# Kernel tuning notes

Measured on AMD Instinct MI355X. Metric: run time of the kernel, lower is better.

Reference implementation:

```python
import jax, jax.numpy as jnp
import numpy as np

B, K, C, D, L, H, FF = 64, 1024, 512, 256, 2, 4, 1024
DH = D // H
EPS = 1e-5
NEG = -jnp.inf
SCALE = 1.0 / float(np.sqrt(DH))


def _ln(x, w, b):
    m = x.mean(-1, keepdims=True)
    v = ((x - m) ** 2).mean(-1, keepdims=True)
    return (x - m) * jax.lax.rsqrt(v + EPS) * w + b


def _star_attn(x, key_pad, pad_c, Wq, bq, Wk, bk, Wv, bv, Wo, bo):
    # Star topology: rows 0,1 (query,dustbin) attend to all non-padded keys;
    # each candidate row attends only to {query, dustbin, itself}.
    Bb, S, _ = x.shape
    q = (x @ Wq.T + bq).reshape(Bb, S, H, DH)
    k = (x @ Wk.T + bk).reshape(Bb, S, H, DH)
    v = (x @ Wv.T + bv).reshape(Bb, S, H, DH)
    # global rows
    qg = q[:, :2]
    sg = jnp.einsum('bthd,bshd->bhts', qg, k) * SCALE            # [B,H,2,S]
    sg = jnp.where(key_pad[:, None, None, :], NEG, sg)
    out_g = jnp.einsum('bhts,bshd->bthd', jax.nn.softmax(sg, -1), v)  # [B,2,H,DH]
    # candidate rows: scores against the 2 global keys + self key
    qc, kc, vc = q[:, 2:], k[:, 2:], v[:, 2:]
    kg, vg = k[:, :2], v[:, :2]
    s2 = jnp.einsum('bkhd,bthd->bkht', qc, kg) * SCALE           # [B,K,H,2]
    ss = jnp.einsum('bkhd,bkhd->bkh', qc, kc) * SCALE            # [B,K,H]
    ss = jnp.where(pad_c[:, :, None], NEG, ss)                   # padded self-key disallowed
    w = jax.nn.softmax(jnp.concatenate([s2, ss[..., None]], -1), -1)  # [B,K,H,3]
    out_c = jnp.einsum('bkht,bthd->bkhd', w[..., :2], vg) + w[..., 2:] * vc
    out = jnp.concatenate([out_g, out_c], 1).reshape(Bb, S, D)
    return out @ Wo.T + bo


def _forward(query, candidates, candidate_mask, qp_w, qp_b, cp_w, cp_b,
             dustbin, type_emb, ln1_w, ln1_b, ln2_w, ln2_b,
             Wq, bq, Wk, bk, Wv, bv, Wo, bo,
             ff1_w, ff1_b, ff2_w, ff2_b, head_ln_w, head_ln_b, head_w, head_b):
    Bb = query.shape[0]
    qt = (query @ qp_w.T + qp_b + type_emb[0])[:, None]          # [B,1,D]
    dt = jnp.broadcast_to(dustbin + type_emb[1], (Bb, 1, D))
    ct = candidates @ cp_w.T + cp_b + type_emb[2]                # [B,K,D]
    x = jnp.concatenate([qt, dt, ct], 1)                         # [B,K+2,D]
    pad_c = jnp.logical_not(candidate_mask)
    key_pad = jnp.concatenate([jnp.zeros((Bb, 2), bool), pad_c], 1)
    for l in range(L):  # pre-LN encoder layers (norm_first, eval so dropout=0)
        x = x + _star_attn(_ln(x, ln1_w[l], ln1_b[l]), key_pad, pad_c,
                           Wq[l], bq[l], Wk[l], bk[l], Wv[l], bv[l], Wo[l], bo[l])
        h = _ln(x, ln2_w[l], ln2_b[l])
        x = x + (jax.nn.gelu(h @ ff1_w[l].T + ff1_b[l], approximate=False) @ ff2_w[l].T + ff2_b[l])
    logits = (_ln(x, head_ln_w, head_ln_b) @ head_w.T + head_b)[..., 0]  # [B,K+2]
    cand = jnp.where(candidate_mask, logits[:, 2:], NEG)
    return jnp.concatenate([logits[:, 1:2], cand], 1)            # [B,K+1]


def setup_inputs() -> dict:
    key = jax.random.key(0)
    ks = iter(jax.random.split(key, 40))
    n = lambda shape, s=0.02: jax.random.normal(next(ks), shape, jnp.float32) * s
    return dict(
        query=jax.random.normal(next(ks), (B, C), jnp.float32),
        candidates=jax.random.normal(next(ks), (B, K, C), jnp.float32),
        candidate_mask=jax.random.bernoulli(next(ks), 0.9, (B, K)),
        qp_w=n((D, C)), qp_b=jnp.zeros(D),
        cp_w=n((D, C)), cp_b=jnp.zeros(D),
        dustbin=n((D,)), type_emb=n((3, D)),
        ln1_w=jnp.ones((L, D)), ln1_b=jnp.zeros((L, D)),
        ln2_w=jnp.ones((L, D)), ln2_b=jnp.zeros((L, D)),
        Wq=n((L, D, D)), bq=jnp.zeros((L, D)),
        Wk=n((L, D, D)), bk=jnp.zeros((L, D)),
        Wv=n((L, D, D)), bv=jnp.zeros((L, D)),
        Wo=n((L, D, D)), bo=jnp.zeros((L, D)),
        ff1_w=n((L, FF, D)), ff1_b=jnp.zeros((L, FF)),
        ff2_w=n((L, D, FF)), ff2_b=jnp.zeros((L, D)),
        head_ln_w=jnp.ones(D), head_ln_b=jnp.zeros(D),
        head_w=n((1, D)), head_b=jnp.zeros(1),
    )


def reference(query, candidates, candidate_mask, qp_w, qp_b, cp_w, cp_b,
              dustbin, type_emb, ln1_w, ln1_b, ln2_w, ln2_b,
              Wq, bq, Wk, bk, Wv, bv, Wo, bo,
              ff1_w, ff1_b, ff2_w, ff2_b, head_ln_w, head_ln_b, head_w, head_b):
    return _forward(query, candidates, candidate_mask, qp_w, qp_b, cp_w, cp_b,
                    dustbin, type_emb, ln1_w, ln1_b, ln2_w, ln2_b,
                    Wq, bq, Wk, bk, Wv, bv, Wo, bo,
                    ff1_w, ff1_b, ff2_w, ff2_b, head_ln_w, head_ln_b, head_w, head_b)
```

## Files before the change

### kernel.cpp

```cpp
#include <hip/hip_runtime.h>
#include <math.h>

static constexpr int Bc = 64;
static constexpr int Kc = 1024;
static constexpr int Cc = 512;
static constexpr int Dc = 256;
static constexpr int Hc = 4;
static constexpr int Sc = 1026;
static constexpr int FFc = 1024;
static constexpr float EPSc = 1e-5f;
static constexpr float SCALEc = 0.125f;
static constexpr float NEG_OUT = -1.0e30f;

typedef __attribute__((ext_vector_type(8))) short short8;
typedef __attribute__((ext_vector_type(8))) unsigned short u16x8;
typedef __attribute__((ext_vector_type(4))) float f32x4;

__device__ __forceinline__ float bf2f(unsigned short u) {
  union { float f; unsigned int i; } c; c.i = ((unsigned int)u) << 16; return c.f;
}
__device__ __forceinline__ unsigned short f2bf(float f) {
  union { float f; unsigned int i; } c; c.f = f;
  unsigned int i = c.i;
  unsigned int r = (i + 0x7fffu + ((i >> 16) & 1u)) >> 16;
  return (unsigned short)r;
}
__device__ __forceinline__ unsigned int cvt_pk_bf16(float a, float b) {
  unsigned int d;
  asm("v_cvt_pk_bf16_f32 %0, %1, %2" : "=v"(d) : "v"(a), "v"(b));
  return d;
}

__device__ __forceinline__ float wave_sum(float v) {
#pragma unroll
  for (int off = 32; off > 0; off >>= 1) v += __shfl_xor(v, off, 64);
  return v;
}
__device__ __forceinline__ float wave_max(float v) {
#pragma unroll
  for (int off = 32; off > 0; off >>= 1) v = fmaxf(v, __shfl_xor(v, off, 64));
  return v;
}

__device__ __forceinline__ void async_ld16(const unsigned short* g, unsigned short* l) {
  __builtin_amdgcn_global_load_lds(
      (const __attribute__((address_space(1))) void*)g,
      (__attribute__((address_space(3))) void*)l, 16, 0, 0);
}

__device__ __forceinline__ float gelu_fast(float u) {
  const float z = u * fmaf(u * u, 0.07135481627f, 1.5957691216f);
  return __fdividef(u, 1.0f + __expf(-z));
}

template <int EPI, int MAP, int CASTA>
__global__ __launch_bounds__(256) void gemm_mfma(
    const void* __restrict__ Av, const unsigned short* __restrict__ W,
    const float* __restrict__ bias, const void* extra,
    void* Cout, int N, int Kd, int ldc, int MB, int NB) {
  __shared__ unsigned short lds[24576];
  const int xcd = blockIdx.x & 7;
  const int slot = blockIdx.x >> 3;
  const int nb = slot % NB;
  const int mb = (slot / NB) * 8 + xcd;
  if (mb >= MB) return;
  const int m0 = mb * 128;
  const int n0 = nb * 128;
  const int tid = threadIdx.x;
  const int w = tid >> 6;
  const int lane = tid & 63;

  const unsigned short* A = (const unsigned short*)Av;
  const float* Af = (const float*)Av;

  const int srA[2] = {(w * 2 + 0) * 16 + (lane >> 2), (w * 2 + 1) * 16 + (lane >> 2)};
  const unsigned short* pA[2];
  const unsigned short* pB[2];
#pragma unroll
  for (int c = 0; c < 2; ++c) {
    const int kc = ((lane & 3) ^ ((srA[c] >> 1) & 3)) * 8;
    if (!CASTA) pA[c] = A + (size_t)(m0 + srA[c]) * Kd + kc;
    pB[c] = W + (size_t)(n0 + srA[c]) * Kd + kc;
  }
  const int lreg0 = (w * 2 + 0) * 512;
  const int lreg1 = (w * 2 + 1) * 512;

  f32x4 zero = {0.f, 0.f, 0.f, 0.f};
  f32x4 acc[4][4];
#pragma unroll
  for (int i = 0; i < 4; ++i)
#pragma unroll
    for (int j = 0; j < 4; ++j) acc[i][j] = zero;

  const int mrow = (w & 1) * 64;
  const int nrow = (w >> 1) * 64;
  const int l15 = lane & 15;
  const int quad = lane >> 4;
  const int koff = (quad ^ ((l15 >> 1) & 3)) * 16;

  auto stage = [&](int kk, int b) {
    if (CASTA) {
#pragma unroll
      for (int wi = 0; wi < 4; ++wi) {
        const int g = wi * 256 + tid;
        const int row = g >> 3;
        const int k4 = g & 7;
        const int phys =
            row * 32 + ((((k4 >> 1) ^ ((row >> 1) & 3))) << 3) + ((k4 & 1) << 2);
        const float4 a4 =
            *(const float4*)(Af + (size_t)(m0 + row) * Kd + kk + k4 * 4);
        uint2 o;
        o.x = cvt_pk_bf16(a4.x, a4.y);
        o.y = cvt_pk_bf16(a4.z, a4.w);
        *(uint2*)(&lds[b * 4096 + phys]) = o;
      }
    } else {
      async_ld16(pA[0] + kk, &lds[b * 4096 + lreg0]);
      async_ld16(pA[1] + kk, &lds[b * 4096 + lreg1]);
    }
    async_ld16(pB[0] + kk, &lds[12288 + b * 4096 + lreg0]);
    async_ld16(pB[1] + kk, &lds[12288 + b * 4096 + lreg1]);
  };

  auto compute_tile = [&](int cur) {
    const char* AsB = (const char*)&lds[cur * 4096];
    const char* WsB = (const char*)&lds[12288 + cur * 4096];
    short8 af[4], bfr[4];
#pragma unroll
    for (int i = 0; i < 4; ++i)
      af[i] = *(const short8*)(AsB + (size_t)(mrow + i * 16 + l15) * 64 + koff);
#pragma unroll
    for (int j = 0; j < 4; ++j)
      bfr[j] = *(const short8*)(WsB + (size_t)(nrow + j * 16 + l15) * 64 + koff);
#pragma unroll
    for (int i = 0; i < 4; ++i)
#pragma unroll
      for (int j = 0; j < 4; ++j)
        acc[i][j] = __builtin_amdgcn_mfma_f32_16x16x32_bf16(bfr[j], af[i],
                                                            acc[i][j], 0, 0, 0);
  };

  const int niter = Kd >> 5;
  if (CASTA) {
    stage(0, 0);
    for (int it = 0; it < niter; ++it) {
      const int cur = it & 1;
      __syncthreads();
      if (it + 1 < niter) stage((it + 1) << 5, cur ^ 1);
      compute_tile(cur);
    }
  } else {
    stage(0, 0);
    stage(32, 1);
    int cur = 0;
    for (int it = 0; it < niter; ++it) {
      if (it + 1 < niter)
        asm volatile("s_waitcnt vmcnt(4)" ::: "memory");
      else
        asm volatile("s_waitcnt vmcnt(0)" ::: "memory");
      asm volatile("s_waitcnt lgkmcnt(0)" ::: "memory");
      __builtin_amdgcn_s_barrier();
      if (it + 2 < niter) {
        int b2 = cur + 2; if (b2 >= 3) b2 -= 3;
        stage((it + 2) << 5, b2);
      }
      compute_tile(cur);
      cur = (cur == 2) ? 0 : cur + 1;
    }
  }

  const float* extraF = (const float*)extra;
  const unsigned short* extraB = (const unsigned short*)extra;
  float4 bj[4];
#pragma unroll
  for (int j = 0; j < 4; ++j) {
    const int n = n0 + nrow + j * 16 + quad * 4;
    float4 t4 = *(const float4*)(bias + n);
    if (EPI == 1) {
      const float4 e4 = *(const float4*)(extraF + n);
      t4.x += e4.x; t4.y += e4.y; t4.z += e4.z; t4.w += e4.w;
    }
    bj[j] = t4;
  }
  __syncthreads();
#pragma unroll
  for (int i = 0; i < 4; ++i) {
    const int m = mrow + i * 16 + l15;
    const int swz = (m & 7) << 1;
#pragma unroll
    for (int j = 0; j < 4; ++j) {
      float v0 = acc[i][j][0] + bj[j].x;
      float v1 = acc[i][j][1] + bj[j].y;
      float v2 = acc[i][j][2] + bj[j].z;
      float v3 = acc[i][j][3] + bj[j].w;
      if (EPI == 3) {
        v0 = gelu_fast(v0); v1 = gelu_fast(v1);
        v2 = gelu_fast(v2); v3 = gelu_fast(v3);
      }
      uint2 pk;
      pk.x = cvt_pk_bf16(v0, v1);
      pk.y = cvt_pk_bf16(v2, v3);
      const int g = ((nrow + j * 16 + quad * 4) >> 2) ^ swz;
      *(uint2*)(&lds[m * 128 + g * 4]) = pk;
    }
  }
  __syncthreads();
  unsigned short* outb = (unsigned short*)Cout;
#pragma unroll
  for (int c8 = 0; c8 < 8; ++c8) {
    const int idx = c8 * 256 + tid;
    const int row = idx >> 4;
    const int cc = idx & 15;
    const int gsr = (2 * cc) ^ ((row & 7) << 1);
    u16x8 val = *(const u16x8*)(&lds[row * 128 + gsr * 4]);
    const int col = cc * 8;
    const int m = m0 + row;
    const size_t orow =
        (MAP == 1) ? ((size_t)(m >> 10) * Sc + 2 + (m & 1023)) : (size_t)m;
    const size_t go = orow * (size_t)ldc + n0 + col;
    if (EPI == 2) {
      u16x8 rv = *(const u16x8*)(extraB + go);
      unsigned int* vp = (unsigned int*)&val;
#pragma unroll
      for (int e = 0; e < 4; ++e) {
        const float a0 = bf2f(val[2 * e]) + bf2f(rv[2 * e]);
        const float a1 = bf2f(val[2 * e + 1]) + bf2f(rv[2 * e + 1]);
        vp[e] = cvt_pk_bf16(a0, a1);
      }
    }
    *(u16x8*)(outb + go) = val;
  }
}

struct CastTab {
  const float* src[10];
  unsigned short* dst[10];
  int n4[10];
};
__global__ __launch_bounds__(256) void cast_multi(CastTab t) {
  const int e = blockIdx.y;
  const int n4 = t.n4[e];
  const float4* s = (const float4*)t.src[e];
  uint2* d = (uint2*)t.dst[e];
  for (int i = blockIdx.x * 256 + threadIdx.x; i < n4; i += gridDim.x * 256) {
    float4 f = s[i];
    uint2 o;
    o.x = cvt_pk_bf16(f.x, f.y);
    o.y = cvt_pk_bf16(f.z, f.w);
    d[i] = o;
  }
}

__global__ __launch_bounds__(256) void bias_concat(const float* bq, const float* bk,
                                                   const float* bv, float* qkvb) {
  const int i = blockIdx.x * 256 + threadIdx.x;
  if (i >= 2 * 768) return;
  const int l = i / 768;
  const int j = i - l * 768;
  float v;
  if (j < 256) v = bq[l * 256 + j];
  else if (j < 512) v = bk[l * 256 + j - 256];
  else v = bv[l * 256 + j - 512];
  qkvb[i] = v;
}

__global__ __launch_bounds__(256) void embed_qd(
    const float* __restrict__ qin, const float* __restrict__ qp_w,
    const float* __restrict__ qp_b, const float* __restrict__ dustbin,
    const float* __restrict__ type_emb, unsigned short* __restrict__ x) {
  const int b = blockIdx.x;
  const int d = threadIdx.x;
  __shared__ __align__(16) float qs[512];
  qs[d] = qin[b * 512 + d];
  qs[d + 256] = qin[b * 512 + 256 + d];
  __syncthreads();
  float acc = 0.0f;
  const float* wr = qp_w + (size_t)d * 512;
#pragma unroll 4
  for (int c = 0; c < 512; c += 4) {
    float4 w4 = *(const float4*)(wr + c);
    acc = fmaf(qs[c], w4.x, acc);
    acc = fmaf(qs[c + 1], w4.y, acc);
    acc = fmaf(qs[c + 2], w4.z, acc);
    acc = fmaf(qs[c + 3], w4.w, acc);
  }
  const size_t base = (size_t)b * Sc * Dc;
  x[base + d] = f2bf(acc + qp_b[d] + type_emb[d]);
  x[base + Dc + d] = f2bf(dustbin[d] + type_emb[Dc + d]);
}

__global__ __launch_bounds__(256) void ln_kernel(
    const unsigned short* __restrict__ x, const float* __restrict__ w,
    const float* __restrict__ b, unsigned short* __restrict__ y, int nrows) {
  const int wave = threadIdx.x >> 6;
  const int lane = threadIdx.x & 63;
  const int row0 = blockIdx.x * 16 + wave * 4;
  const float4 wv = *(const float4*)(w + lane * 4);
  const float4 bv = *(const float4*)(b + lane * 4);
#pragma unroll
  for (int r = 0; r < 4; ++r) {
    const int row = row0 + r;
    if (row >= nrows) return;
    const unsigned short* xr = x + (size_t)row * Dc;
    ushort4 xv = *(const ushort4*)(xr + lane * 4);
    const float v0 = bf2f(xv.x), v1 = bf2f(xv.y), v2 = bf2f(xv.z), v3 = bf2f(xv.w);
    float s = v0 + v1 + v2 + v3;
    float sq = v0 * v0 + v1 * v1 + v2 * v2 + v3 * v3;
    s = wave_sum(s);
    sq = wave_sum(sq);
    const float mean = s * (1.0f / Dc);
    const float var = sq * (1.0f / Dc) - mean * mean;
    const float rs = rsqrtf(var + EPSc);
    uint2 o;
    o.x = cvt_pk_bf16((v0 - mean) * rs * wv.x + bv.x,
                      (v1 - mean) * rs * wv.y + bv.y);
    o.y = cvt_pk_bf16((v2 - mean) * rs * wv.z + bv.z,
                      (v3 - mean) * rs * wv.w + bv.w);
    *(uint2*)(y + (size_t)row * Dc + lane * 4) = o;
  }
}

__global__ __launch_bounds__(256) void attn_global(
    const unsigned short* __restrict__ qkv, const unsigned char* __restrict__ mask,
    unsigned short* __restrict__ ao) {
  const int b = blockIdx.x;
  const int h = blockIdx.y;
  const int tid = threadIdx.x;
  const int wv = tid >> 6;
  const int lane = tid & 63;
  __shared__ float q0s[64], q1s[64];
  __shared__ float sc0[Sc], sc1[Sc];
  __shared__ float rbuf[4][2];
  __shared__ float obuf[2][4][64];
  const size_t base = (size_t)b * Sc * 768 + h * 64;
  if (tid < 64) {
    q0s[tid] = bf2f(qkv[base + tid]);
    q1s[tid] = bf2f(qkv[base + 768 + tid]);
  }
  __syncthreads();

  float lm0 = -INFINITY, lm1 = -INFINITY;
  for (int s = tid; s < Sc; s += 256) {
    const unsigned short* kr = qkv + base + 256 + (size_t)s * 768;
    float d0 = 0.0f, d1 = 0.0f;
#pragma unroll
    for (int c = 0; c < 64; c += 8) {
      u16x8 kv = *(const u16x8*)(kr + c);
#pragma unroll
      for (int e = 0; e < 8; ++e) {
        const float kf = bf2f(kv[e]);
        d0 = fmaf(q0s[c + e], kf, d0);
        d1 = fmaf(q1s[c + e], kf, d1);
      }
    }
    const bool pad = (s >= 2) && (mask[b * Kc + (s - 2)] == 0);
    const float s0 = pad ? -INFINITY : d0 * SCALEc;
    const float s1 = pad ? -INFINITY : d1 * SCALEc;
    sc0[s] = s0; sc1[s] = s1;
    lm0 = fmaxf(lm0, s0); lm1 = fmaxf(lm1, s1);
  }
  lm0 = wave_max(lm0);
  lm1 = wave_max(lm1);
  if (lane == 0) { rbuf[wv][0] = lm0; rbuf[wv][1] = lm1; }
  __syncthreads();
  const float m0 = fmaxf(fmaxf(rbuf[0][0], rbuf[1][0]), fmaxf(rbuf[2][0], rbuf[3][0]));
  const float m1 = fmaxf(fmaxf(rbuf[0][1], rbuf[1][1]), fmaxf(rbuf[2][1], rbuf[3][1]));
  float ls0 = 0.0f, ls1 = 0.0f;
  for (int s = tid; s < Sc; s += 256) {
    const float e0 = expf(sc0[s] - m0);
    const float e1 = expf(sc1[s] - m1);
    sc0[s] = e0; sc1[s] = e1;
    ls0 += e0; ls1 += e1;
  }
  ls0 = wave_sum(ls0);
  ls1 = wave_sum(ls1);
  __syncthreads();
  if (lane == 0) { rbuf[wv][0] = ls0; rbuf[wv][1] = ls1; }
  __syncthreads();
  const float t0 = rbuf[0][0] + rbuf[1][0] + rbuf[2][0] + rbuf[3][0];
  const float t1 = rbuf[0][1] + rbuf[1][1] + rbuf[2][1] + rbuf[3][1];
  float o0 = 0.0f, o1 = 0.0f;
  for (int s = wv; s < Sc; s += 4) {
    const float vvv = bf2f(qkv[base + 512 + (size_t)s * 768 + lane]);
    o0 = fmaf(sc0[s], vvv, o0);
    o1 = fmaf(sc1[s], vvv, o1);
  }
  obuf[0][wv][lane] = o0;
  obuf[1][wv][lane] = o1;
  __syncthreads();
  if (wv == 0) {
    const float a0 = obuf[0][0][lane] + obuf[0][1][lane] + obuf[0][2][lane] + obuf[0][3][lane];
    const float a1 = obuf[1][0][lane] + obuf[1][1][lane] + obuf[1][2][lane] + obuf[1][3][lane];
    const size_t ob = ((size_t)b * Sc) * Dc + h * 64;
    ao[ob + lane] = f2bf(a0 / t0);
    ao[ob + Dc + lane] = f2bf(a1 / t1);
  }
}

__global__ __launch_bounds__(256) void attn_cand(
    const unsigned short* __restrict__ qkv, const unsigned char* __restrict__ mask,
    unsigned short* __restrict__ ao) {
  const int b = blockIdx.x >> 3;
  const int k0 = (blockIdx.x & 7) << 7;
  const int h = threadIdx.x >> 6;
  const int lane = threadIdx.x & 63;
  const int c4 = lane >> 4;
  const int l16 = lane & 15;
  const size_t bbase = (size_t)b * Sc * 768;
  const unsigned short* gp = qkv + bbase + h * 64 + l16 * 4;
  float k0f[4], k1f[4], v0f[4], v1f[4];
  {
    const ushort4 a = *(const ushort4*)(gp + 256);
    const ushort4 c = *(const ushort4*)(gp + 256 + 768);
    const ushort4 d = *(const ushort4*)(gp + 512);
    const ushort4 e = *(const ushort4*)(gp + 512 + 768);
    k0f[0] = bf2f(a.x); k0f[1] = bf2f(a.y); k0f[2] = bf2f(a.z); k0f[3] = bf2f(a.w);
    k1f[0] = bf2f(c.x); k1f[1] = bf2f(c.y); k1f[2] = bf2f(c.z); k1f[3] = bf2f(c.w);
    v0f[0] = bf2f(d.x); v0f[1] = bf2f(d.y); v0f[2] = bf2f(d.z); v0f[3] = bf2f(d.w);
    v1f[0] = bf2f(e.x); v1f[1] = bf2f(e.y); v1f[2] = bf2f(e.z); v1f[3] = bf2f(e.w);
  }
  for (int t = 0; t < 32; ++t) {
    const int kk = k0 + t * 4 + c4;
    const unsigned short* cp =
        qkv + bbase + (size_t)(2 + kk) * 768 + h * 64 + l16 * 4;
    const ushort4 qv = *(const ushort4*)cp;
    const ushort4 kv = *(const ushort4*)(cp + 256);
    const ushort4 vv = *(const ushort4*)(cp + 512);
    const unsigned short* qp = (const unsigned short*)&qv;
    const unsigned short* kp = (const unsigned short*)&kv;
    const unsigned short* vp = (const unsigned short*)&vv;
    float p0 = 0.f, p1 = 0.f, p2 = 0.f;
#pragma unroll
    for (int e = 0; e < 4; ++e) {
      const float qf = bf2f(qp[e]);
      p0 = fmaf(qf, k0f[e], p0);
      p1 = fmaf(qf, k1f[e], p1);
      p2 = fmaf(qf, bf2f(kp[e]), p2);
    }
#pragma unroll
    for (int off = 1; off < 16; off <<= 1) {
      p0 += __shfl_xor(p0, off, 64);
      p1 += __shfl_xor(p1, off, 64);
      p2 += __shfl_xor(p2, off, 64);
    }
    const bool pad = (mask[b * Kc + kk] == 0);
    const float s0 = p0 * SCALEc;
    const float s1 = p1 * SCALEc;
    const float s2 = pad ? -INFINITY : p2 * SCALEc;
    const float m = fmaxf(fmaxf(s0, s1), s2);
    const float e0 = expf(s0 - m);
    const float e1 = expf(s1 - m);
    const float e2 = pad ? 0.0f : expf(s2 - m);
    const float inv = 1.0f / (e0 + e1 + e2);
    float o[4];
#pragma unroll
    for (int e = 0; e < 4; ++e)
      o[e] = (e0 * v0f[e] + e1 * v1f[e] + e2 * bf2f(vp[e])) * inv;
    uint2 pk;
    pk.x = cvt_pk_bf16(o[0], o[1]);
    pk.y = cvt_pk_bf16(o[2], o[3]);
    *(uint2*)(ao + ((size_t)b * Sc + 2 + kk) * Dc + h * 64 + l16 * 4) = pk;
  }
}

__global__ __launch_bounds__(256) void head_kernel(
    const unsigned short* __restrict__ x, const float* __restrict__ lnw,
    const float* __restrict__ lnb, const float* __restrict__ hw,
    const float* __restrict__ hb, const unsigned char* __restrict__ mask,
    float* __restrict__ out) {
  const int lane = threadIdx.x & 63;
  const int gw0 = blockIdx.x * 16 + (threadIdx.x >> 6) * 4;
  const float4 wv = *(const float4*)(lnw + lane * 4);
  const float4 bv = *(const float4*)(lnb + lane * 4);
  const float4 hv = *(const float4*)(hw + lane * 4);
  const float hb0 = hb[0];
#pragma unroll
  for (int r = 0; r < 4; ++r) {
    const int gw = gw0 + r;
    if (gw >= Bc * 1025) return;
    const int b = gw / 1025;
    const int j = gw - b * 1025;
    const int s = 1 + j;
    const unsigned short* xr = x + ((size_t)b * Sc + s) * Dc;
    ushort4 xv = *(const ushort4*)(xr + lane * 4);
    const float v0 = bf2f(xv.x), v1 = bf2f(xv.y), v2 = bf2f(xv.z), v3 = bf2f(xv.w);
    float su = v0 + v1 + v2 + v3;
    float sq = v0 * v0 + v1 * v1 + v2 * v2 + v3 * v3;
    su = wave_sum(su);
    sq = wave_sum(sq);
    const float mean = su * (1.0f / Dc);
    const float var = sq * (1.0f / Dc) - mean * mean;
    const float rs = rsqrtf(var + EPSc);
    float d = ((v0 - mean) * rs * wv.x + bv.x) * hv.x +
              ((v1 - mean) * rs * wv.y + bv.y) * hv.y +
              ((v2 - mean) * rs * wv.z + bv.z) * hv.z +
              ((v3 - mean) * rs * wv.w + bv.w) * hv.w;
    d = wave_sum(d);
    if (lane == 0) {
      const float logit = d + hb0;
      float res;
      if (j == 0) res = logit;
      else res = (mask[b * Kc + (j - 1)] != 0) ? logit : NEG_OUT;
      out[(size_t)b * 1025 + j] = res;
    }
  }
}

extern "C" void kernel_launch(void* const* d_in, const int* in_sizes, int n_in,
                              void* d_out, int out_size, void* d_ws,
                              size_t ws_size, hipStream_t stream) {
  const float* query = (const float*)d_in[0];
  const float* cands = (const float*)d_in[1];
  const unsigned char* mask = (const unsigned char*)d_in[2];
  const float* qp_w = (const float*)d_in[3];
  const float* qp_b = (const float*)d_in[4];
  const float* cp_w = (const float*)d_in[5];
  const float* cp_b = (const float*)d_in[6];
  const float* dustbin = (const float*)d_in[7];
  const float* type_emb = (const float*)d_in[8];
  const float* ln1_w = (const float*)d_in[9];
  const float* ln1_b = (const float*)d_in[10];
  const float* ln2_w = (const float*)d_in[11];
  const float* ln2_b = (const float*)d_in[12];
  const float* Wq = (const float*)d_in[13];
  const float* bq = (const float*)d_in[14];
  const float* Wk = (const float*)d_in[15];
  const float* bk = (const float*)d_in[16];
  const float* Wv = (const float*)d_in[17];
  const float* bv = (const float*)d_in[18];
  const float* Wo = (const float*)d_in[19];
  const float* bo = (const float*)d_in[20];
  const float* f1w = (const float*)d_in[21];
  const float* f1b = (const float*)d_in[22];
  const float* f2w = (const float*)d_in[23];
  const float* f2b = (const float*)d_in[24];
  const float* hlw = (const float*)d_in[25];
  const float* hlb = (const float*)d_in[26];
  const float* hw = (const float*)d_in[27];
  const float* hb = (const float*)d_in[28];
  float* out = (float*)d_out;

  const size_t XSZ = (size_t)Bc * Sc * Dc;
  const size_t FFSZ = (size_t)Bc * Sc * FFc;

  char* p = (char*)d_ws;
  unsigned short* x = (unsigned short*)p;   p += XSZ * 2;
  unsigned short* y = (unsigned short*)p;   p += XSZ * 2;
  unsigned short* ao = (unsigned short*)p;  p += XSZ * 2;
  unsigned short* big = (unsigned short*)p; p += FFSZ * 2;
  unsigned short* qkv = big;
  unsigned short* ff = big;
  unsigned short* cpw_b = (unsigned short*)p;
  unsigned short* qkvw_b = cpw_b + 131072;
  unsigned short* Wo_b = qkvw_b + 2 * 768 * 256;
  unsigned short* f1_b = Wo_b + 131072;
  unsigned short* f2_b = f1_b + 524288;
  float* qkvb = (float*)(f2_b + 524288);

  const int BS = Bc * Sc;
  auto sgrid = [](int MB, int NB) { return (unsigned)(NB * (((MB + 7) >> 3) << 3)); };

  CastTab t;
  t.src[0] = cp_w;  t.dst[0] = cpw_b; t.n4[0] = 131072 / 4;
  t.src[1] = Wo;    t.dst[1] = Wo_b;  t.n4[1] = 131072 / 4;
  t.src[2] = f1w;   t.dst[2] = f1_b;  t.n4[2] = 524288 / 4;
  t.src[3] = f2w;   t.dst[3] = f2_b;  t.n4[3] = 524288 / 4;
  for (int l = 0; l < 2; ++l) {
    t.src[4 + l * 3 + 0] = Wq + l * 65536;
    t.src[4 + l * 3 + 1] = Wk + l * 65536;
    t.src[4 + l * 3 + 2] = Wv + l * 65536;
    t.dst[4 + l * 3 + 0] = qkvw_b + l * 196608 + 0 * 65536;
    t.dst[4 + l * 3 + 1] = qkvw_b + l * 196608 + 1 * 65536;
    t.dst[4 + l * 3 + 2] = qkvw_b + l * 196608 + 2 * 65536;
    t.n4[4 + l * 3 + 0] = 65536 / 4;
    t.n4[4 + l * 3 + 1] = 65536 / 4;
    t.n4[4 + l * 3 + 2] = 65536 / 4;
  }
  cast_multi<<<dim3(128, 10), 256, 0, stream>>>(t);
  bias_concat<<<6, 256, 0, stream>>>(bq, bk, bv, qkvb);

  gemm_mfma<1, 1, 1><<<sgrid(512, 2), 256, 0, stream>>>(
      cands, cpw_b, cp_b, type_emb + 2 * Dc, x, Dc, Cc, Dc, 512, 2);
  embed_qd<<<Bc, 256, 0, stream>>>(query, qp_w, qp_b, dustbin, type_emb, x);

  for (int l = 0; l < 2; ++l) {
    ln_kernel<<<(BS + 15) / 16, 256, 0, stream>>>(x, ln1_w + l * Dc, ln1_b + l * Dc, y, BS);
    gemm_mfma<4, 0, 0><<<sgrid(513, 6), 256, 0, stream>>>(
        y, qkvw_b + l * 196608, qkvb + l * 768, nullptr, qkv, 768, Dc, 768, 513, 6);
    attn_global<<<dim3(Bc, Hc), 256, 0, stream>>>(qkv, mask, ao);
    attn_cand<<<Bc * 8, 256, 0, stream>>>(qkv, mask, ao);
    gemm_mfma<2, 0, 0><<<sgrid(513, 2), 256, 0, stream>>>(
        ao, Wo_b + l * 65536, bo + l * Dc, x, x, Dc, Dc, Dc, 513, 2);
    ln_kernel<<<(BS + 15) / 16, 256, 0, stream>>>(x, ln2_w + l * Dc, ln2_b + l * Dc, y, BS);
    gemm_mfma<3, 0, 0><<<sgrid(513, 8), 256, 0, stream>>>(
        y, f1_b + l * 524288 / 2, f1b + l * FFc, nullptr, ff, FFc, Dc, FFc, 513, 8);
    gemm_mfma<2, 0, 0><<<sgrid(513, 2), 256, 0, stream>>>(
        ff, f2_b + l * 524288 / 2, f2b + l * Dc, x, x, Dc, FFc, Dc, 513, 2);
  }

  head_kernel<<<(Bc * 1025 + 15) / 16, 256, 0, stream>>>(x, hlw, hlb, hw, hb, mask, out);
}
```

Baseline: 956.2 us.

## Fuse attention kernels, preload bias into accumulators, unroll pipeline, cheaper GELU exp

```diff
diff --git a/kernel.cpp b/kernel.cpp
--- a/kernel.cpp
+++ b/kernel.cpp
@@ -49,8 +49,10 @@
 }
 
 __device__ __forceinline__ float gelu_fast(float u) {
-  const float z = u * fmaf(u * u, 0.07135481627f, 1.5957691216f);
-  return __fdividef(u, 1.0f + __expf(-z));
+  const float m = fmaf(u * u, -0.10294916f, -2.3021174f);
+  float e;
+  asm("v_exp_f32 %0, %1" : "=v"(e) : "v"(u * m));
+  return __fdividef(u, 1.0f + e);
 }
 
 template <int EPI, int MAP, int CASTA>
@@ -85,18 +87,32 @@
   const int lreg0 = (w * 2 + 0) * 512;
   const int lreg1 = (w * 2 + 1) * 512;
 
-  f32x4 zero = {0.f, 0.f, 0.f, 0.f};
-  f32x4 acc[4][4];
-#pragma unroll
-  for (int i = 0; i < 4; ++i)
-#pragma unroll
-    for (int j = 0; j < 4; ++j) acc[i][j] = zero;
-
   const int mrow = (w & 1) * 64;
   const int nrow = (w >> 1) * 64;
   const int l15 = lane & 15;
   const int quad = lane >> 4;
   const int koff = (quad ^ ((l15 >> 1) & 3)) * 16;
+
+  const float* extraF = (const float*)extra;
+  float4 bj[4];
+#pragma unroll
+  for (int j = 0; j < 4; ++j) {
+    const int n = n0 + nrow + j * 16 + quad * 4;
+    float4 t4 = *(const float4*)(bias + n);
+    if (EPI == 1) {
+      const float4 e4 = *(const float4*)(extraF + n);
+      t4.x += e4.x; t4.y += e4.y; t4.z += e4.z; t4.w += e4.w;
+    }
+    bj[j] = t4;
+  }
+  f32x4 acc[4][4];
+#pragma unroll
+  for (int i = 0; i < 4; ++i)
+#pragma unroll
+    for (int j = 0; j < 4; ++j) {
+      acc[i][j][0] = bj[j].x; acc[i][j][1] = bj[j].y;
+      acc[i][j][2] = bj[j].z; acc[i][j][3] = bj[j].w;
+    }
 
   auto stage = [&](int kk, int b) {
     if (CASTA) {
@@ -152,8 +168,7 @@
   } else {
     stage(0, 0);
     stage(32, 1);
-    int cur = 0;
-    for (int it = 0; it < niter; ++it) {
+    auto step = [&](int it, int c) {
       if (it + 1 < niter)
         asm volatile("s_waitcnt vmcnt(4)" ::: "memory");
       else
@@ -161,27 +176,21 @@
       asm volatile("s_waitcnt lgkmcnt(0)" ::: "memory");
       __builtin_amdgcn_s_barrier();
       if (it + 2 < niter) {
-        int b2 = cur + 2; if (b2 >= 3) b2 -= 3;
+        int b2 = c + 2; if (b2 >= 3) b2 -= 3;
         stage((it + 2) << 5, b2);
       }
-      compute_tile(cur);
-      cur = (cur == 2) ? 0 : cur + 1;
-    }
-  }
-
-  const float* extraF = (const float*)extra;
+      compute_tile(c);
+    };
+    int it = 0;
+    for (; it + 3 <= niter; it += 3) {
+      step(it + 0, 0);
+      step(it + 1, 1);
+      step(it + 2, 2);
+    }
+    for (; it < niter; ++it) step(it, it % 3);
+  }
+
   const unsigned short* extraB = (const unsigned short*)extra;
-  float4 bj[4];
-#pragma unroll
-  for (int j = 0; j < 4; ++j) {
-    const int n = n0 + nrow + j * 16 + quad * 4;
-    float4 t4 = *(const float4*)(bias + n);
-    if (EPI == 1) {
-      const float4 e4 = *(const float4*)(extraF + n);
-      t4.x += e4.x; t4.y += e4.y; t4.z += e4.z; t4.w += e4.w;
-    }
-    bj[j] = t4;
-  }
   __syncthreads();
 #pragma unroll
   for (int i = 0; i < 4; ++i) {
@@ -189,10 +198,10 @@
     const int swz = (m & 7) << 1;
 #pragma unroll
     for (int j = 0; j < 4; ++j) {
-      float v0 = acc[i][j][0] + bj[j].x;
-      float v1 = acc[i][j][1] + bj[j].y;
-      float v2 = acc[i][j][2] + bj[j].z;
-      float v3 = acc[i][j][3] + bj[j].w;
+      float v0 = acc[i][j][0];
+      float v1 = acc[i][j][1];
+      float v2 = acc[i][j][2];
+      float v3 = acc[i][j][3];
       if (EPI == 3) {
         v0 = gelu_fast(v0); v1 = gelu_fast(v1);
         v2 = gelu_fast(v2); v3 = gelu_fast(v3);
@@ -320,90 +329,91 @@
   }
 }
 
-__global__ __launch_bounds__(256) void attn_global(
+__global__ __launch_bounds__(256) void attn_fused(
     const unsigned short* __restrict__ qkv, const unsigned char* __restrict__ mask,
     unsigned short* __restrict__ ao) {
-  const int b = blockIdx.x;
-  const int h = blockIdx.y;
-  const int tid = threadIdx.x;
-  const int wv = tid >> 6;
-  const int lane = tid & 63;
   __shared__ float q0s[64], q1s[64];
   __shared__ float sc0[Sc], sc1[Sc];
   __shared__ float rbuf[4][2];
   __shared__ float obuf[2][4][64];
-  const size_t base = (size_t)b * Sc * 768 + h * 64;
-  if (tid < 64) {
-    q0s[tid] = bf2f(qkv[base + tid]);
-    q1s[tid] = bf2f(qkv[base + 768 + tid]);
-  }
-  __syncthreads();
-
-  float lm0 = -INFINITY, lm1 = -INFINITY;
-  for (int s = tid; s < Sc; s += 256) {
-    const unsigned short* kr = qkv + base + 256 + (size_t)s * 768;
-    float d0 = 0.0f, d1 = 0.0f;
-#pragma unroll
-    for (int c = 0; c < 64; c += 8) {
-      u16x8 kv = *(const u16x8*)(kr + c);
-#pragma unroll
-      for (int e = 0; e < 8; ++e) {
-        const float kf = bf2f(kv[e]);
-        d0 = fmaf(q0s[c + e], kf, d0);
-        d1 = fmaf(q1s[c + e], kf, d1);
+  const int tid = threadIdx.x;
+
+  if (blockIdx.x < (unsigned)(Bc * Hc)) {
+    const int b = blockIdx.x >> 2;
+    const int h = blockIdx.x & 3;
+    const int wv = tid >> 6;
+    const int lane = tid & 63;
+    const size_t base = (size_t)b * Sc * 768 + h * 64;
+    if (tid < 64) {
+      q0s[tid] = bf2f(qkv[base + tid]);
+      q1s[tid] = bf2f(qkv[base + 768 + tid]);
+    }
+    __syncthreads();
+
+    float lm0 = -INFINITY, lm1 = -INFINITY;
+    for (int s = tid; s < Sc; s += 256) {
+      const unsigned short* kr = qkv + base + 256 + (size_t)s * 768;
+      float d0 = 0.0f, d1 = 0.0f;
+#pragma unroll
+      for (int c = 0; c < 64; c += 8) {
+        u16x8 kv = *(const u16x8*)(kr + c);
+#pragma unroll
+        for (int e = 0; e < 8; ++e) {
+          const float kf = bf2f(kv[e]);
+          d0 = fmaf(q0s[c + e], kf, d0);
+          d1 = fmaf(q1s[c + e], kf, d1);
+        }
       }
-    }
-    const bool pad = (s >= 2) && (mask[b * Kc + (s - 2)] == 0);
-    const float s0 = pad ? -INFINITY : d0 * SCALEc;
-    const float s1 = pad ? -INFINITY : d1 * SCALEc;
-    sc0[s] = s0; sc1[s] = s1;
-    lm0 = fmaxf(lm0, s0); lm1 = fmaxf(lm1, s1);
-  }
-  lm0 = wave_max(lm0);
-  lm1 = wave_max(lm1);
-  if (lane == 0) { rbuf[wv][0] = lm0; rbuf[wv][1] = lm1; }
-  __syncthreads();
-  const float m0 = fmaxf(fmaxf(rbuf[0][0], rbuf[1][0]), fmaxf(rbuf[2][0], rbuf[3][0]));
-  const float m1 = fmaxf(fmaxf(rbuf[0][1], rbuf[1][1]), fmaxf(rbuf[2][1], rbuf[3][1]));
-  float ls0 = 0.0f, ls1 = 0.0f;
-  for (int s = tid; s < Sc; s += 256) {
-    const float e0 = expf(sc0[s] - m0);
-    const float e1 = expf(sc1[s] - m1);
-    sc0[s] = e0; sc1[s] = e1;
-    ls0 += e0; ls1 += e1;
-  }
-  ls0 = wave_sum(ls0);
-  ls1 = wave_sum(ls1);
-  __syncthreads();
-  if (lane == 0) { rbuf[wv][0] = ls0; rbuf[wv][1] = ls1; }
-  __syncthreads();
-  const float t0 = rbuf[0][0] + rbuf[1][0] + rbuf[2][0] + rbuf[3][0];
-  const float t1 = rbuf[0][1] + rbuf[1][1] + rbuf[2][1] + rbuf[3][1];
-  float o0 = 0.0f, o1 = 0.0f;
-  for (int s = wv; s < Sc; s += 4) {
-    const float vvv = bf2f(qkv[base + 512 + (size_t)s * 768 + lane]);
-    o0 = fmaf(sc0[s], vvv, o0);
-    o1 = fmaf(sc1[s], vvv, o1);
-  }
-  obuf[0][wv][lane] = o0;
-  obuf[1][wv][lane] = o1;
-  __syncthreads();
-  if (wv == 0) {
-    const float a0 = obuf[0][0][lane] + obuf[0][1][lane] + obuf[0][2][lane] + obuf[0][3][lane];
-    const float a1 = obuf[1][0][lane] + obuf[1][1][lane] + obuf[1][2][lane] + obuf[1][3][lane];
-    const size_t ob = ((size_t)b * Sc) * Dc + h * 64;
-    ao[ob + lane] = f2bf(a0 / t0);
-    ao[ob + Dc + lane] = f2bf(a1 / t1);
-  }
-}
-
-__global__ __launch_bounds__(256) void attn_cand(
-    const unsigned short* __restrict__ qkv, const unsigned char* __restrict__ mask,
-    unsigned short* __restrict__ ao) {
-  const int b = blockIdx.x >> 3;
-  const int k0 = (blockIdx.x & 7) << 7;
-  const int h = threadIdx.x >> 6;
-  const int lane = threadIdx.x & 63;
+      const bool pad = (s >= 2) && (mask[b * Kc + (s - 2)] == 0);
+      const float s0 = pad ? -INFINITY : d0 * SCALEc;
+      const float s1 = pad ? -INFINITY : d1 * SCALEc;
+      sc0[s] = s0; sc1[s] = s1;
+      lm0 = fmaxf(lm0, s0); lm1 = fmaxf(lm1, s1);
+    }
+    lm0 = wave_max(lm0);
+    lm1 = wave_max(lm1);
+    if (lane == 0) { rbuf[wv][0] = lm0; rbuf[wv][1] = lm1; }
+    __syncthreads();
+    const float m0 = fmaxf(fmaxf(rbuf[0][0], rbuf[1][0]), fmaxf(rbuf[2][0], rbuf[3][0]));
+    const float m1 = fmaxf(fmaxf(rbuf[0][1], rbuf[1][1]), fmaxf(rbuf[2][1], rbuf[3][1]));
+    float ls0 = 0.0f, ls1 = 0.0f;
+    for (int s = tid; s < Sc; s += 256) {
+      const float e0 = expf(sc0[s] - m0);
+      const float e1 = expf(sc1[s] - m1);
+      sc0[s] = e0; sc1[s] = e1;
+      ls0 += e0; ls1 += e1;
+    }
+    ls0 = wave_sum(ls0);
+    ls1 = wave_sum(ls1);
+    __syncthreads();
+    if (lane == 0) { rbuf[wv][0] = ls0; rbuf[wv][1] = ls1; }
+    __syncthreads();
+    const float t0 = rbuf[0][0] + rbuf[1][0] + rbuf[2][0] + rbuf[3][0];
+    const float t1 = rbuf[0][1] + rbuf[1][1] + rbuf[2][1] + rbuf[3][1];
+    float o0 = 0.0f, o1 = 0.0f;
+    for (int s = wv; s < Sc; s += 4) {
+      const float vvv = bf2f(qkv[base + 512 + (size_t)s * 768 + lane]);
+      o0 = fmaf(sc0[s], vvv, o0);
+      o1 = fmaf(sc1[s], vvv, o1);
+    }
+    obuf[0][wv][lane] = o0;
+    obuf[1][wv][lane] = o1;
+    __syncthreads();
+    if (wv == 0) {
+      const float a0 = obuf[0][0][lane] + obuf[0][1][lane] + obuf[0][2][lane] + obuf[0][3][lane];
+      const float a1 = obuf[1][0][lane] + obuf[1][1][lane] + obuf[1][2][lane] + obuf[1][3][lane];
+      const size_t ob = ((size_t)b * Sc) * Dc + h * 64;
+      ao[ob + lane] = f2bf(a0 / t0);
+      ao[ob + Dc + lane] = f2bf(a1 / t1);
+    }
+    return;
+  }
+
+  const int bk2 = blockIdx.x - Bc * Hc;
+  const int b = bk2 >> 3;
+  const int k0 = (bk2 & 7) << 7;
+  const int h = tid >> 6;
+  const int lane = tid & 63;
   const int c4 = lane >> 4;
   const int l16 = lane & 15;
   const size_t bbase = (size_t)b * Sc * 768;
@@ -587,8 +597,7 @@
     ln_kernel<<<(BS + 15) / 16, 256, 0, stream>>>(x, ln1_w + l * Dc, ln1_b + l * Dc, y, BS);
     gemm_mfma<4, 0, 0><<<sgrid(513, 6), 256, 0, stream>>>(
         y, qkvw_b + l * 196608, qkvb + l * 768, nullptr, qkv, 768, Dc, 768, 513, 6);
-    attn_global<<<dim3(Bc, Hc), 256, 0, stream>>>(qkv, mask, ao);
-    attn_cand<<<Bc * 8, 256, 0, stream>>>(qkv, mask, ao);
+    attn_fused<<<Bc * Hc + Bc * 8, 256, 0, stream>>>(qkv, mask, ao);
     gemm_mfma<2, 0, 0><<<sgrid(513, 2), 256, 0, stream>>>(
         ao, Wo_b + l * 65536, bo + l * Dc, x, x, Dc, Dc, Dc, 513, 2);
     ln_kernel<<<(BS + 15) / 16, 256, 0, stream>>>(x, ln2_w + l * Dc, ln2_b + l * Dc, y, BS);
```

Result: faster. 902.6 us (-5.6%).
